# Kernel optimization log

Measured on AMD Instinct MI355X. Metric: run time of the kernel, lower is better.

The kernel has to match this reference:

```python
import jax, jax.numpy as jnp
import numpy as np


def setup_inputs() -> dict:
    key = jax.random.key(0)
    k1, k2, k3, k4 = jax.random.split(key, 4)
    B, Tv, Ta, D = 8, 2048, 2048, 256
    return {
        "visual_features": jax.random.normal(k1, (B, Tv, D), dtype=jnp.float32),
        "audio_features": jax.random.normal(k2, (B, Ta, D), dtype=jnp.float32),
        "visual_weights": jax.random.uniform(k3, (D, D), dtype=jnp.float32),
        "audio_weights": jax.random.uniform(k4, (D, D), dtype=jnp.float32),
        "num_neighbors": 8,
    }


def _pairwise_l2(vm, am):
    # ||v - a|| via the expanded form to avoid the [B,Tv,Ta,D] intermediate.
    sq = (
        jnp.sum(vm * vm, -1)[:, :, None]
        + jnp.sum(am * am, -1)[:, None, :]
        - 2.0 * jnp.einsum("btd,bsd->bts", vm, am)
    )
    sq = jnp.maximum(sq, 0.0)
    # safe sqrt: subgradient 0 at 0 (matches torch.norm backward convention)
    return jnp.where(sq > 0, jnp.sqrt(jnp.where(sq > 0, sq, 1.0)), 0.0)


def reference(visual_features, audio_features, visual_weights, audio_weights, num_neighbors):
    vm = visual_features @ visual_weights  # [B,Tv,D]
    am = audio_features @ audio_weights    # [B,Ta,D]
    graph = jnp.exp(-_pairwise_l2(vm, am))  # [B,Tv,Ta]
    # topk over the visual axis (dim=1): move it last for lax.top_k
    _, idx = jax.lax.top_k(jnp.swapaxes(graph, 1, 2), num_neighbors)  # [B,Ta,k]
    idx = jnp.swapaxes(idx, 1, 2)  # [B,k,Ta]
    # broadcasted gather along axis 1: result [B,k,Ta,D]
    vn = jnp.take_along_axis(visual_features[:, :, None, :], idx[..., None], axis=1)
    an = jnp.take_along_axis(audio_features[:, :, None, :], idx[..., None], axis=1)
    # mean over dim=2 (the Ta axis of the gathered neighbors) -> [B,k,D]
    return vn.mean(axis=2), an.mean(axis=2)
```

## Files before the change

kernel.cpp:

```cpp
#include <hip/hip_runtime.h>
#include <cstddef>
#include <cstdint>

namespace {
constexpr int kB   = 8;
constexpr int kT   = 2048;
constexpr int kD   = 256;
constexpr int kK   = 8;
constexpr int kM   = kB * kT;
constexpr int kNC  = kB * kT;
constexpr int kColCap = 64;
constexpr int kOvCap  = 1 << 17;
constexpr int kStr = 264;
constexpr float kMinNormalF = 1.17549435e-38f;
}

typedef __attribute__((ext_vector_type(8)))  __bf16 bf16x8;
typedef __attribute__((ext_vector_type(16))) float  f32x16;

__device__ inline unsigned short f2bf_rne(float x) {
  unsigned u = __float_as_uint(x);
  unsigned r = (u + 0x7FFFu + ((u >> 16) & 1u)) >> 16;
  return (unsigned short)r;
}
__device__ inline float bf2f(unsigned short h) {
  return __uint_as_float((unsigned)h << 16);
}
union FragU { uint4 u4; bf16x8 v; };

__device__ inline void async16(const unsigned short* g, unsigned short* l) {
  __builtin_amdgcn_global_load_lds(
      (const __attribute__((address_space(1))) unsigned int*)(const void*)g,
      (__attribute__((address_space(3))) unsigned int*)(void*)l, 16, 0, 0);
}

__device__ inline void stage_tile_async(const unsigned short* src,
                                        unsigned short* S, int w, int lane) {
  const int hi = lane >> 5, lo = lane & 31;
#pragma unroll
  for (int i = 0; i < 8; ++i) {
    const int p = w * 8 + i;
    const int rowl = p * 2 + hi;
    const int c = lo ^ (rowl & 31);
    async16(src + (size_t)rowl * kD + c * 8, S + p * 512);
  }
}
__device__ inline uint4 lds_frag(const unsigned short* S, int row, int kc, int half) {
  const int c = (kc * 2 + half) ^ (row & 31);
  return *reinterpret_cast<const uint4*>(S + row * 256 + c * 8);
}

__global__ __launch_bounds__(256) void prep(const float* __restrict__ W0,
                                            const float* __restrict__ W1,
                                            unsigned short* __restrict__ T0,
                                            unsigned short* __restrict__ T1,
                                            unsigned* __restrict__ zeroBase,
                                            int zeroWords,
                                            unsigned* __restrict__ outW) {
  const int blk = blockIdx.x;
  if (blk < 128) {
    const float* W = (blk & 64) ? W1 : W0;
    unsigned short* WT = (blk & 64) ? T1 : T0;
    const int t = blk & 63;
    const int c0 = (t & 7) * 32, k0 = (t >> 3) * 32;
    __shared__ float tile[32][33];
    const int tx = threadIdx.x & 31, ty = threadIdx.x >> 5;
#pragma unroll
    for (int i = 0; i < 4; ++i)
      tile[ty + i * 8][tx] = W[(size_t)(k0 + ty + i * 8) * kD + c0 + tx];
    __syncthreads();
#pragma unroll
    for (int i = 0; i < 4; ++i)
      WT[(size_t)(c0 + ty + i * 8) * kD + k0 + tx] = f2bf_rne(tile[tx][ty + i * 8]);
  } else {
    for (int i = (blk - 128) * 256 + threadIdx.x; i < zeroWords; i += 32 * 256)
      zeroBase[i] = 0u;
    for (int i = (blk - 128) * 256 + threadIdx.x; i < 2 * kB * kK * kD; i += 32 * 256)
      outW[i] = 0u;
  }
}

__global__ __launch_bounds__(256) void gemm_hyb(const float* __restrict__ Xv,
                                                const float* __restrict__ Xa,
                                                const unsigned short* __restrict__ WvT,
                                                const unsigned short* __restrict__ WaT,
                                                unsigned short* __restrict__ Cv,
                                                unsigned short* __restrict__ Ca,
                                                float* __restrict__ nv,
                                                float* __restrict__ na) {
  __shared__ unsigned short S[64 * kStr + 64 * 256];
  unsigned short* bufA = S;
  unsigned short* bufB = S + 64 * kStr;
  const int z = blockIdx.z;
  const float* X = z ? Xa : Xv;
  const unsigned short* WT = z ? WaT : WvT;
  unsigned short* Cb = z ? Ca : Cv;
  float* nrm = z ? na : nv;
  const int r0 = blockIdx.x * 64;
  const int tid = threadIdx.x;
  const int w = tid >> 6, lane = tid & 63;
  const int wt = w & 1, wc = w >> 1;
  const int half = lane >> 5, ln = lane & 31;

#pragma unroll
  for (int i = 0; i < 16; ++i) {
    const int idx = i * 256 + tid;
    const int row = idx >> 6, g = idx & 63;
    const float4 v = *reinterpret_cast<const float4*>(X + (size_t)(r0 + row) * kD + g * 4);
    ushort4 o;
    o.x = f2bf_rne(v.x); o.y = f2bf_rne(v.y); o.z = f2bf_rne(v.z); o.w = f2bf_rne(v.w);
    *reinterpret_cast<ushort4*>(bufA + row * kStr + g * 4) = o;
  }
  __syncthreads();

  stage_tile_async(WT, bufB, w, lane);
  uint4 afr[16];
#pragma unroll
  for (int kc = 0; kc < 16; ++kc)
    afr[kc] = *reinterpret_cast<const uint4*>(bufA + (wt * 32 + ln) * kStr + kc * 16 + half * 8);
  __syncthreads();

  float ns[16];
#pragma unroll
  for (int r = 0; r < 16; ++r) ns[r] = 0.0f;

  for (int ct = 0; ct < 4; ++ct) {
    unsigned short* cur = (ct & 1) ? bufA : bufB;
    unsigned short* nxt = (ct & 1) ? bufB : bufA;
    if (ct < 3)
      stage_tile_async(WT + (size_t)(ct + 1) * 64 * kD, nxt, w, lane);
    const int c0 = ct * 64;
    f32x16 acc;
#pragma unroll
    for (int i = 0; i < 16; ++i) acc[i] = 0.0f;
#pragma unroll
    for (int kc = 0; kc < 16; ++kc) {
      FragU fa, fb;
      fa.u4 = afr[kc];
      fb.u4 = lds_frag(cur, wc * 32 + ln, kc, half);
      acc = __builtin_amdgcn_mfma_f32_32x32x16_bf16(fa.v, fb.v, acc, 0, 0, 0);
    }
    const int col = c0 + wc * 32 + ln;
#pragma unroll
    for (int r = 0; r < 16; ++r) {
      const int row = r0 + wt * 32 + (r & 3) + 8 * (r >> 2) + 4 * half;
      const unsigned short us = f2bf_rne(acc[r]);
      Cb[(size_t)row * kD + col] = us;
      const float f = bf2f(us);
      ns[r] += f * f;
    }
    if (ct < 3) __syncthreads();
  }
#pragma unroll
  for (int r = 0; r < 16; ++r) {
    float v = ns[r];
#pragma unroll
    for (int off = 1; off < 32; off <<= 1) v += __shfl_xor(v, off, 64);
    if (ln == 0) {
      const int row = r0 + wt * 32 + (r & 3) + 8 * (r >> 2) + 4 * half;
      atomicAdd(nrm + row, v);
    }
  }
}

__global__ __launch_bounds__(256) void keys_v15(const unsigned short* __restrict__ vmb,
                                                const unsigned short* __restrict__ amb,
                                                const float* __restrict__ vn2,
                                                const float* __restrict__ an2,
                                                unsigned* __restrict__ colCount,
                                                uint2* __restrict__ colRecs,
                                                unsigned* __restrict__ ovCount,
                                                uint2* __restrict__ ovRecs) {
  __shared__ unsigned short S[2][64 * 256];
  const int hw = blockIdx.x + (blockIdx.y << 4) + (blockIdx.z << 7);
  const int lg = ((hw & 7) << 7) | (hw >> 3);
  const int b = lg >> 7;
  const int t0 = (lg & 15) << 7;
  const int sr0 = ((lg >> 4) & 7) << 8;
  const int tid = threadIdx.x;
  const int w = tid >> 6, lane = tid & 63;
  const int half = lane >> 5, ln = lane & 31;

  stage_tile_async(vmb + ((size_t)b * kT + t0) * kD, S[0], w, lane);
  stage_tile_async(vmb + ((size_t)b * kT + t0 + 64) * kD, S[1], w, lane);
  __syncthreads();
  uint4 afr[16];
  {
    const unsigned short* Sa = S[w >> 1];
#pragma unroll
    for (int kc = 0; kc < 16; ++kc)
      afr[kc] = lds_frag(Sa, (w & 1) * 32 + ln, kc, half);
  }
  __syncthreads();

  stage_tile_async(amb + ((size_t)b * kT + sr0) * kD, S[0], w, lane);
  __syncthreads();

  const float* v2p = vn2 + (size_t)b * kT + t0 + w * 32;

  for (int st = 0; st < 4; ++st) {
    const int s0 = sr0 + st * 64;
    const int cur = st & 1;
    if (st < 3)
      stage_tile_async(amb + ((size_t)b * kT + s0 + 64) * kD, S[cur ^ 1], w, lane);
    f32x16 acc[2];
#pragma unroll
    for (int j = 0; j < 2; ++j)
#pragma unroll
      for (int i = 0; i < 16; ++i) acc[j][i] = 0.0f;
#pragma unroll
    for (int kc = 0; kc < 16; ++kc) {
      FragU fa; fa.u4 = afr[kc];
#pragma unroll
      for (int ss = 0; ss < 2; ++ss) {
        FragU fb;
        fb.u4 = lds_frag(S[cur], ss * 32 + ln, kc, half);
        acc[ss] = __builtin_amdgcn_mfma_f32_32x32x16_bf16(fa.v, fb.v, acc[ss], 0, 0, 0);
      }
    }
    float a2s[2];
#pragma unroll
    for (int ss = 0; ss < 2; ++ss)
      a2s[ss] = an2[(size_t)b * kT + s0 + ss * 32 + ln];
#pragma unroll
    for (int g = 0; g < 4; ++g) {
      const float4 v2 = *reinterpret_cast<const float4*>(v2p + g * 8 + half * 4);
      const float v2a[4] = {v2.x, v2.y, v2.z, v2.w};
#pragma unroll
      for (int ss = 0; ss < 2; ++ss) {
        const int s = s0 + ss * 32 + ln;
        const float a2 = a2s[ss];
        const int c = (b << 11) | s;
#pragma unroll
        for (int q = 0; q < 4; ++q) {
          const float raw = v2a[q] + a2 - 2.0f * acc[ss][4 * g + q];
          if (raw < 7744.0f) {
            const float dist = sqrtf(fmaxf(raw, 0.0f));
            const float e = expf(-dist);
            if (e >= kMinNormalF) {
              const int t = t0 + w * 32 + g * 8 + half * 4 + q;
              const unsigned slot = atomicAdd(&colCount[c], 1u);
              if (slot < (unsigned)kColCap) {
                colRecs[(size_t)c * kColCap + slot] = make_uint2(__float_as_uint(e), (unsigned)t);
              } else {
                const unsigned pos = ((unsigned)b << 22) | ((unsigned)s << 11) | (unsigned)t;
                const unsigned oi = atomicAdd(ovCount, 1u);
                if (oi < (unsigned)kOvCap) ovRecs[oi] = make_uint2(__float_as_uint(e), pos);
              }
            }
          }
        }
      }
    }
    if (st < 3) __syncthreads();
  }
}

__global__ __launch_bounds__(1024) void finalize_hist(const unsigned* __restrict__ colCount,
                                                      const uint2* __restrict__ colRecs,
                                                      const unsigned* __restrict__ ovCount,
                                                      const uint2* __restrict__ ovRecs,
                                                      unsigned* __restrict__ hist) {
  __shared__ unsigned lhist[kT * kK];
  const int b = blockIdx.x;
  const int tid = threadIdx.x;
#pragma unroll
  for (int i = 0; i < kT * kK / 1024; ++i)
    lhist[i * 1024 + tid] = 0u;
  __syncthreads();

  for (int s = tid; s < kT; s += 1024) {
    const int c = (b << 11) | s;
    unsigned K[8]; int T[8];
#pragma unroll
    for (int i = 0; i < 8; ++i) { K[i] = 0u; T[i] = 0x7FFFFFFF; }
    const int cnt = (int)colCount[c];
    const int m = min(cnt, kColCap);
    for (int i = 0; i < m; ++i) {
      const uint2 r = colRecs[(size_t)c * kColCap + i];
      const unsigned kx = r.x; const int tx = (int)r.y;
      if (kx > K[7] || (kx == K[7] && tx < T[7])) {
        K[7] = kx; T[7] = tx;
#pragma unroll
        for (int q = 7; q >= 1; --q) {
          const bool sw = (K[q] > K[q - 1]) || (K[q] == K[q - 1] && T[q] < T[q - 1]);
          if (sw) {
            const unsigned tk = K[q]; K[q] = K[q - 1]; K[q - 1] = tk;
            const int tt = T[q];      T[q] = T[q - 1]; T[q - 1] = tt;
          }
        }
      }
    }
    if (cnt > kColCap) {
      int n = (int)*ovCount;
      if (n > kOvCap) n = kOvCap;
      for (int i = 0; i < n; ++i) {
        const uint2 r = ovRecs[i];
        if ((int)(r.y >> 11) == c) {
          const unsigned kx = r.x; const int tx = (int)(r.y & 2047u);
          if (kx > K[7] || (kx == K[7] && tx < T[7])) {
            K[7] = kx; T[7] = tx;
#pragma unroll
            for (int q = 7; q >= 1; --q) {
              const bool sw = (K[q] > K[q - 1]) || (K[q] == K[q - 1] && T[q] < T[q - 1]);
              if (sw) {
                const unsigned tk = K[q]; K[q] = K[q - 1]; K[q - 1] = tk;
                const int tt = T[q];      T[q] = T[q - 1]; T[q - 1] = tt;
              }
            }
          }
        }
      }
    }
    int mcnt = 0;
#pragma unroll
    for (int i = 0; i < 8; ++i) if (K[i] > 0u) mcnt++;
    int outv[8];
#pragma unroll
    for (int i = 0; i < 8; ++i) outv[i] = T[i];
    int cand = 0;
    for (int r = mcnt; r < 8; ++r) {
      bool taken = true;
      while (taken) {
        taken = false;
#pragma unroll
        for (int q = 0; q < 8; ++q)
          if (q < mcnt && T[q] == cand) taken = true;
        if (taken) cand++;
      }
      outv[r] = cand++;
    }
#pragma unroll
    for (int j = 0; j < 8; ++j)
      atomicAdd(&lhist[(outv[j] << 3) + j], 1u);
  }
  __syncthreads();
  unsigned* hb = hist + ((size_t)b << 11) * kK;
#pragma unroll
  for (int i = 0; i < kT * kK / 1024; ++i)
    hb[i * 1024 + tid] = lhist[i * 1024 + tid];
}

__global__ __launch_bounds__(256) void wsum(const float* __restrict__ visual,
                                            const float* __restrict__ audio,
                                            const unsigned* __restrict__ hist,
                                            float* __restrict__ out) {
  __shared__ unsigned hs[64 * kK];
  const int b = blockIdx.y;
  const int t0 = blockIdx.x * 64;
  const int d = threadIdx.x;
  const size_t hbase = (((size_t)b << 11) + t0) * kK;
  hs[d] = hist[hbase + d];
  hs[d + 256] = hist[hbase + d + 256];
  __syncthreads();
  float accV[8], accA[8];
#pragma unroll
  for (int j = 0; j < 8; ++j) { accV[j] = 0.f; accA[j] = 0.f; }
  const size_t xbase = ((size_t)b * kT + t0) * kD + d;
  for (int i = 0; i < 64; ++i) {
    const float v = visual[xbase + (size_t)i * kD];
    const float a = audio[xbase + (size_t)i * kD];
#pragma unroll
    for (int j = 0; j < 8; ++j) {
      const float cf = (float)hs[i * kK + j];
      accV[j] += cf * v;
      accA[j] += cf * a;
    }
  }
#pragma unroll
  for (int j = 0; j < 8; ++j) {
    const size_t bj = (size_t)b * kK + j;
    atomicAdd(&out[bj * kD + d], accV[j] * (1.0f / kT));
    atomicAdd(&out[(size_t)kB * kK * kD + bj * kD + d], accA[j] * (1.0f / kT));
  }
}

extern "C" void kernel_launch(void* const* d_in, const int* in_sizes, int n_in,
                              void* d_out, int out_size, void* d_ws, size_t ws_size,
                              hipStream_t stream) {
  (void)in_sizes; (void)n_in; (void)out_size; (void)ws_size;
  const float* visual = (const float*)d_in[0];
  const float* audio  = (const float*)d_in[1];
  const float* Wv     = (const float*)d_in[2];
  const float* Wa     = (const float*)d_in[3];
  float* out = (float*)d_out;

  char* ws = (char*)d_ws;
  unsigned short* WvT = (unsigned short*)ws;
  unsigned short* WaT = WvT + (size_t)kD * kD;
  unsigned short* vmb = WaT + (size_t)kD * kD;
  unsigned short* amb = vmb + (size_t)kM * kD;
  float* vn2 = (float*)(amb + (size_t)kM * kD);
  float* an2 = vn2 + kM;
  unsigned* colCount = (unsigned*)(an2 + kM);
  unsigned* ovCount  = colCount + kNC;
  unsigned* hist     = ovCount + 8;
  uint2* colRecs = (uint2*)(hist + (size_t)kM * kK);
  uint2* ovRecs  = colRecs + (size_t)kNC * kColCap;
  const int zeroWords = 2 * kM + kNC + 8;

  prep<<<dim3(160), 256, 0, stream>>>(Wv, Wa, WvT, WaT, (unsigned*)vn2, zeroWords,
                                      (unsigned*)out);
  gemm_hyb<<<dim3(kM / 64, 1, 2), 256, 0, stream>>>(visual, audio, WvT, WaT,
                                                    vmb, amb, vn2, an2);
  keys_v15<<<dim3(kT / 128, kT / 256, kB), 256, 0, stream>>>(vmb, amb, vn2, an2,
                                                             colCount, colRecs, ovCount, ovRecs);
  finalize_hist<<<dim3(kB), 1024, 0, stream>>>(colCount, colRecs, ovCount,
                                               ovRecs, hist);
  wsum<<<dim3(kT / 64, kB), 256, 0, stream>>>(visual, audio, hist, out);
}
```

Before: 153.5 us.

## Fuse histogram finalize with weighted sum via flag-based producer/consumer blocks

Merges finalize_hist and wsum into one kernel. The first 8 blocks build per-batch histograms and publish a release flag; the other 256 blocks prefetch their visual/audio rows to warm the cache, spin on the flag, then do the weighted sum. This removes a launch boundary and overlaps the input loads with the serial top-k finalize. Separately, the keys kernel gives each block 512 audio columns instead of 256, halving the grid and reusing the visual fragments in registers over more tiles. Risks: the finalize now runs on 256 threads instead of 1024, and the spin-wait can deadlock if the producer blocks are not scheduled while consumers occupy every CU.

```diff
diff --git a/kernel.cpp b/kernel.cpp
--- a/kernel.cpp
+++ b/kernel.cpp
@@ -163,7 +163,7 @@
   }
 }
 
-__global__ __launch_bounds__(256) void keys_v15(const unsigned short* __restrict__ vmb,
+__global__ __launch_bounds__(256) void keys_v18(const unsigned short* __restrict__ vmb,
                                                 const unsigned short* __restrict__ amb,
                                                 const float* __restrict__ vn2,
                                                 const float* __restrict__ an2,
@@ -172,11 +172,11 @@
                                                 unsigned* __restrict__ ovCount,
                                                 uint2* __restrict__ ovRecs) {
   __shared__ unsigned short S[2][64 * 256];
-  const int hw = blockIdx.x + (blockIdx.y << 4) + (blockIdx.z << 7);
-  const int lg = ((hw & 7) << 7) | (hw >> 3);
-  const int b = lg >> 7;
+  const int hw = blockIdx.x + (blockIdx.y << 4) + (blockIdx.z << 6);
+  const int lg = ((hw & 7) << 6) | (hw >> 3);
+  const int b = lg >> 6;
   const int t0 = (lg & 15) << 7;
-  const int sr0 = ((lg >> 4) & 7) << 8;
+  const int sr0 = ((lg >> 4) & 3) << 9;
   const int tid = threadIdx.x;
   const int w = tid >> 6, lane = tid & 63;
   const int half = lane >> 5, ln = lane & 31;
@@ -198,10 +198,10 @@
 
   const float* v2p = vn2 + (size_t)b * kT + t0 + w * 32;
 
-  for (int st = 0; st < 4; ++st) {
+  for (int st = 0; st < 8; ++st) {
     const int s0 = sr0 + st * 64;
     const int cur = st & 1;
-    if (st < 3)
+    if (st < 7)
       stage_tile_async(amb + ((size_t)b * kT + s0 + 64) * kD, S[cur ^ 1], w, lane);
     f32x16 acc[2];
 #pragma unroll
@@ -252,126 +252,137 @@
         }
       }
     }
-    if (st < 3) __syncthreads();
-  }
-}
-
-__global__ __launch_bounds__(1024) void finalize_hist(const unsigned* __restrict__ colCount,
-                                                      const uint2* __restrict__ colRecs,
-                                                      const unsigned* __restrict__ ovCount,
-                                                      const uint2* __restrict__ ovRecs,
-                                                      unsigned* __restrict__ hist) {
+    if (st < 7) __syncthreads();
+  }
+}
+
+__global__ __launch_bounds__(256) void finwsum(const unsigned* __restrict__ colCount,
+                                               const uint2* __restrict__ colRecs,
+                                               const unsigned* __restrict__ ovCount,
+                                               const uint2* __restrict__ ovRecs,
+                                               unsigned* __restrict__ hist,
+                                               unsigned* __restrict__ flags,
+                                               const float* __restrict__ visual,
+                                               const float* __restrict__ audio,
+                                               float* __restrict__ out) {
   __shared__ unsigned lhist[kT * kK];
-  const int b = blockIdx.x;
   const int tid = threadIdx.x;
-#pragma unroll
-  for (int i = 0; i < kT * kK / 1024; ++i)
-    lhist[i * 1024 + tid] = 0u;
-  __syncthreads();
-
-  for (int s = tid; s < kT; s += 1024) {
-    const int c = (b << 11) | s;
-    unsigned K[8]; int T[8];
-#pragma unroll
-    for (int i = 0; i < 8; ++i) { K[i] = 0u; T[i] = 0x7FFFFFFF; }
-    const int cnt = (int)colCount[c];
-    const int m = min(cnt, kColCap);
-    for (int i = 0; i < m; ++i) {
-      const uint2 r = colRecs[(size_t)c * kColCap + i];
-      const unsigned kx = r.x; const int tx = (int)r.y;
-      if (kx > K[7] || (kx == K[7] && tx < T[7])) {
-        K[7] = kx; T[7] = tx;
-#pragma unroll
-        for (int q = 7; q >= 1; --q) {
-          const bool sw = (K[q] > K[q - 1]) || (K[q] == K[q - 1] && T[q] < T[q - 1]);
-          if (sw) {
-            const unsigned tk = K[q]; K[q] = K[q - 1]; K[q - 1] = tk;
-            const int tt = T[q];      T[q] = T[q - 1]; T[q - 1] = tt;
+  if (blockIdx.x < 8) {
+    const int b = blockIdx.x;
+    for (int i = tid; i < kT * kK; i += 256) lhist[i] = 0u;
+    __syncthreads();
+    for (int s = tid; s < kT; s += 256) {
+      const int c = (b << 11) | s;
+      unsigned K[8]; int T[8];
+#pragma unroll
+      for (int i = 0; i < 8; ++i) { K[i] = 0u; T[i] = 0x7FFFFFFF; }
+      const int cnt = (int)colCount[c];
+      const int m = min(cnt, kColCap);
+      for (int i = 0; i < m; ++i) {
+        const uint2 r = colRecs[(size_t)c * kColCap + i];
+        const unsigned kx = r.x; const int tx = (int)r.y;
+        if (kx > K[7] || (kx == K[7] && tx < T[7])) {
+          K[7] = kx; T[7] = tx;
+#pragma unroll
+          for (int q = 7; q >= 1; --q) {
+            const bool sw = (K[q] > K[q - 1]) || (K[q] == K[q - 1] && T[q] < T[q - 1]);
+            if (sw) {
+              const unsigned tk = K[q]; K[q] = K[q - 1]; K[q - 1] = tk;
+              const int tt = T[q];      T[q] = T[q - 1]; T[q - 1] = tt;
+            }
           }
         }
       }
-    }
-    if (cnt > kColCap) {
-      int n = (int)*ovCount;
-      if (n > kOvCap) n = kOvCap;
-      for (int i = 0; i < n; ++i) {
-        const uint2 r = ovRecs[i];
-        if ((int)(r.y >> 11) == c) {
-          const unsigned kx = r.x; const int tx = (int)(r.y & 2047u);
-          if (kx > K[7] || (kx == K[7] && tx < T[7])) {
-            K[7] = kx; T[7] = tx;
-#pragma unroll
-            for (int q = 7; q >= 1; --q) {
-              const bool sw = (K[q] > K[q - 1]) || (K[q] == K[q - 1] && T[q] < T[q - 1]);
-              if (sw) {
-                const unsigned tk = K[q]; K[q] = K[q - 1]; K[q - 1] = tk;
-                const int tt = T[q];      T[q] = T[q - 1]; T[q - 1] = tt;
+      if (cnt > kColCap) {
+        int n = (int)*ovCount;
+        if (n > kOvCap) n = kOvCap;
+        for (int i = 0; i < n; ++i) {
+          const uint2 r = ovRecs[i];
+          if ((int)(r.y >> 11) == c) {
+            const unsigned kx = r.x; const int tx = (int)(r.y & 2047u);
+            if (kx > K[7] || (kx == K[7] && tx < T[7])) {
+              K[7] = kx; T[7] = tx;
+#pragma unroll
+              for (int q = 7; q >= 1; --q) {
+                const bool sw = (K[q] > K[q - 1]) || (K[q] == K[q - 1] && T[q] < T[q - 1]);
+                if (sw) {
+                  const unsigned tk = K[q]; K[q] = K[q - 1]; K[q - 1] = tk;
+                  const int tt = T[q];      T[q] = T[q - 1]; T[q - 1] = tt;
+                }
               }
             }
           }
         }
       }
-    }
-    int mcnt = 0;
-#pragma unroll
-    for (int i = 0; i < 8; ++i) if (K[i] > 0u) mcnt++;
-    int outv[8];
-#pragma unroll
-    for (int i = 0; i < 8; ++i) outv[i] = T[i];
-    int cand = 0;
-    for (int r = mcnt; r < 8; ++r) {
-      bool taken = true;
-      while (taken) {
-        taken = false;
-#pragma unroll
-        for (int q = 0; q < 8; ++q)
-          if (q < mcnt && T[q] == cand) taken = true;
-        if (taken) cand++;
-      }
-      outv[r] = cand++;
-    }
-#pragma unroll
-    for (int j = 0; j < 8; ++j)
-      atomicAdd(&lhist[(outv[j] << 3) + j], 1u);
-  }
-  __syncthreads();
-  unsigned* hb = hist + ((size_t)b << 11) * kK;
-#pragma unroll
-  for (int i = 0; i < kT * kK / 1024; ++i)
-    hb[i * 1024 + tid] = lhist[i * 1024 + tid];
-}
-
-__global__ __launch_bounds__(256) void wsum(const float* __restrict__ visual,
-                                            const float* __restrict__ audio,
-                                            const unsigned* __restrict__ hist,
-                                            float* __restrict__ out) {
-  __shared__ unsigned hs[64 * kK];
-  const int b = blockIdx.y;
-  const int t0 = blockIdx.x * 64;
-  const int d = threadIdx.x;
-  const size_t hbase = (((size_t)b << 11) + t0) * kK;
-  hs[d] = hist[hbase + d];
-  hs[d + 256] = hist[hbase + d + 256];
-  __syncthreads();
-  float accV[8], accA[8];
-#pragma unroll
-  for (int j = 0; j < 8; ++j) { accV[j] = 0.f; accA[j] = 0.f; }
-  const size_t xbase = ((size_t)b * kT + t0) * kD + d;
-  for (int i = 0; i < 64; ++i) {
-    const float v = visual[xbase + (size_t)i * kD];
-    const float a = audio[xbase + (size_t)i * kD];
+      int mcnt = 0;
+#pragma unroll
+      for (int i = 0; i < 8; ++i) if (K[i] > 0u) mcnt++;
+      int outv[8];
+#pragma unroll
+      for (int i = 0; i < 8; ++i) outv[i] = T[i];
+      int cand = 0;
+      for (int r = mcnt; r < 8; ++r) {
+        bool taken = true;
+        while (taken) {
+          taken = false;
+#pragma unroll
+          for (int q = 0; q < 8; ++q)
+            if (q < mcnt && T[q] == cand) taken = true;
+          if (taken) cand++;
+        }
+        outv[r] = cand++;
+      }
+#pragma unroll
+      for (int j = 0; j < 8; ++j)
+        atomicAdd(&lhist[(outv[j] << 3) + j], 1u);
+    }
+    __syncthreads();
+    unsigned* hb = hist + ((size_t)b << 11) * kK;
+    for (int i = tid; i < kT * kK; i += 256)
+      __hip_atomic_store(&hb[i], lhist[i], __ATOMIC_RELAXED, __HIP_MEMORY_SCOPE_AGENT);
+    __threadfence();
+    __syncthreads();
+    if (tid == 0)
+      __hip_atomic_store(&flags[b], 1u, __ATOMIC_RELEASE, __HIP_MEMORY_SCOPE_AGENT);
+  } else {
+    const int u = (int)blockIdx.x - 8;
+    const int b = u >> 5;
+    const int t0 = (u & 31) * 64;
+    const int d = tid;
+    const size_t xbase = ((size_t)b * kT + t0) * kD + d;
+    float warm = 0.f;
+    for (int i = 0; i < 64; ++i)
+      warm += visual[xbase + (size_t)i * kD] + audio[xbase + (size_t)i * kD];
+    asm volatile("" :: "v"(warm));
+    if (tid == 0) {
+      while (__hip_atomic_load(&flags[b], __ATOMIC_ACQUIRE,
+                               __HIP_MEMORY_SCOPE_AGENT) == 0u)
+        __builtin_amdgcn_s_sleep(8);
+    }
+    __syncthreads();
+    const unsigned* hsrc = hist + (((size_t)b << 11) + t0) * kK;
+    lhist[d] = __hip_atomic_load(&hsrc[d], __ATOMIC_RELAXED, __HIP_MEMORY_SCOPE_AGENT);
+    lhist[d + 256] = __hip_atomic_load(&hsrc[d + 256], __ATOMIC_RELAXED, __HIP_MEMORY_SCOPE_AGENT);
+    __syncthreads();
+    float accV[8], accA[8];
+#pragma unroll
+    for (int j = 0; j < 8; ++j) { accV[j] = 0.f; accA[j] = 0.f; }
+    for (int i = 0; i < 64; ++i) {
+      const float v = visual[xbase + (size_t)i * kD];
+      const float a = audio[xbase + (size_t)i * kD];
+#pragma unroll
+      for (int j = 0; j < 8; ++j) {
+        const float cf = (float)lhist[i * kK + j];
+        accV[j] += cf * v;
+        accA[j] += cf * a;
+      }
+    }
 #pragma unroll
     for (int j = 0; j < 8; ++j) {
-      const float cf = (float)hs[i * kK + j];
-      accV[j] += cf * v;
-      accA[j] += cf * a;
-    }
-  }
-#pragma unroll
-  for (int j = 0; j < 8; ++j) {
-    const size_t bj = (size_t)b * kK + j;
-    atomicAdd(&out[bj * kD + d], accV[j] * (1.0f / kT));
-    atomicAdd(&out[(size_t)kB * kK * kD + bj * kD + d], accA[j] * (1.0f / kT));
+      const size_t bj = (size_t)b * kK + j;
+      atomicAdd(&out[bj * kD + d], accV[j] * (1.0f / kT));
+      atomicAdd(&out[(size_t)kB * kK * kD + bj * kD + d], accA[j] * (1.0f / kT));
+    }
   }
 }
 
@@ -394,18 +405,18 @@
   float* an2 = vn2 + kM;
   unsigned* colCount = (unsigned*)(an2 + kM);
   unsigned* ovCount  = colCount + kNC;
-  unsigned* hist     = ovCount + 8;
+  unsigned* flags    = ovCount + 8;
+  unsigned* hist     = flags + 8;
   uint2* colRecs = (uint2*)(hist + (size_t)kM * kK);
   uint2* ovRecs  = colRecs + (size_t)kNC * kColCap;
-  const int zeroWords = 2 * kM + kNC + 8;
+  const int zeroWords = 2 * kM + kNC + 16;
 
   prep<<<dim3(160), 256, 0, stream>>>(Wv, Wa, WvT, WaT, (unsigned*)vn2, zeroWords,
                                       (unsigned*)out);
   gemm_hyb<<<dim3(kM / 64, 1, 2), 256, 0, stream>>>(visual, audio, WvT, WaT,
                                                     vmb, amb, vn2, an2);
-  keys_v15<<<dim3(kT / 128, kT / 256, kB), 256, 0, stream>>>(vmb, amb, vn2, an2,
+  keys_v18<<<dim3(kT / 128, kT / 512, kB), 256, 0, stream>>>(vmb, amb, vn2, an2,
                                                              colCount, colRecs, ovCount, ovRecs);
-  finalize_hist<<<dim3(kB), 1024, 0, stream>>>(colCount, colRecs, ovCount,
-                                               ovRecs, hist);
-  wsum<<<dim3(kT / 64, kB), 256, 0, stream>>>(visual, audio, hist, out);
-}
+  finwsum<<<dim3(8 + 256), 256, 0, stream>>>(colCount, colRecs, ovCount, ovRecs,
+                                             hist, flags, visual, audio, out);
+}
```

Measured after the change: 240.8 us. +56.9%, slower.
